# Optimization experiments

Measured on AMD Instinct MI355X. Metric: run time of the kernel, lower is better.

## Reference

```python
import jax, jax.numpy as jnp
import numpy as np
import math

XLEN, YLEN, B = 2048, 1024, 8
XD, YD, HD, YOUT = 1024, 1024, 512, 1024


def setup_inputs() -> dict:
    key = jax.random.key(0)
    ks = jax.random.split(key, 12)

    def lin(kw, kb, out_d, in_d):
        s = 1.0 / math.sqrt(in_d)
        w = jax.random.uniform(kw, (out_d, in_d), jnp.float32, -s, s)
        b = jax.random.uniform(kb, (out_d,), jnp.float32, -s, s)
        return w, b

    Xk_w, Xk_b = lin(ks[0], ks[1], HD, XD)
    Xv_w, Xv_b = lin(ks[2], ks[3], HD, XD)
    Yq_w, Yq_b = lin(ks[4], ks[5], HD, YD)
    Yw_w, Yw_b = lin(ks[6], ks[7], YOUT, YD + HD)

    X = jax.random.normal(ks[8], (XLEN, B, XD), jnp.float32)
    Y = jax.random.normal(ks[9], (YLEN, B, YD), jnp.float32)
    alignment = jax.random.normal(ks[10], (B, YLEN, XLEN), jnp.float32)
    X_pad_mask = jax.random.bernoulli(ks[11], 0.1, (B, YLEN, XLEN))  # True -> mask out
    align_w = jnp.zeros((1,), jnp.float32)  # nn.Parameter([0])

    return {"X": X, "Y": Y, "alignment": alignment, "X_pad_mask": X_pad_mask,
            "Xk_w": Xk_w, "Xk_b": Xk_b, "Xv_w": Xv_w, "Xv_b": Xv_b,
            "Yq_w": Yq_w, "Yq_b": Yq_b, "Yw_w": Yw_w, "Yw_b": Yw_b,
            "align_w": align_w}


def reference(X, Y, alignment, X_pad_mask, Xk_w, Xk_b, Xv_w, Xv_b,
              Yq_w, Yq_b, Yw_w, Yw_b, align_w):
    FMAX = jnp.finfo(X.dtype).max
    # projections (torch Linear: x @ W.T + b)
    xk = X @ Xk_w.T + Xk_b                     # (x, b, hd)
    yq = Y @ Yq_w.T + Yq_b                     # (y, b, hd)
    # scaled cross-attention logits
    logit = jnp.einsum('xbd,ybd->byx', xk, yq) / math.sqrt(xk.shape[-1])
    # gated alignment bias + clamp
    logit = logit + jax.nn.sigmoid(align_w[0]) * alignment
    logit = jnp.maximum(logit, -FMAX)
    # pad-mask additive fill (-FMAX) then clamp (matches masked_fill + add + clamp)
    logit = jnp.maximum(logit + jnp.where(X_pad_mask, -FMAX, 0.0), -FMAX)
    attn = jax.nn.softmax(logit, axis=-1)      # (b, y, x); dropout = identity (eval)
    xv = X @ Xv_w.T + Xv_b                     # (x, b, hd)
    attn_feat = jnp.einsum('byx,xbh->ybh', attn, xv)  # (y, b, hd)
    concat = jnp.concatenate([Y, attn_feat], axis=-1)  # (y, b, yd+hd)
    return concat @ Yw_w.T + Yw_b              # (y, b, y_outdim)
```

## Files before the change

kernel.cpp:

```cpp
#include <hip/hip_runtime.h>


#define FMAXF 3.402823466e38f

typedef __attribute__((ext_vector_type(8))) __bf16 bf16x8;
typedef __attribute__((ext_vector_type(4))) float f32x4;

static __device__ __forceinline__ short f2b(float f) {
  union { float f; unsigned u; } x; x.f = f;
  unsigned r = (x.u + 0x7FFFu + ((x.u >> 16) & 1u)) >> 16;
  return (short)r;
}
static __device__ __forceinline__ float b2f(short s) {
  union { unsigned u; float f; } x; x.u = ((unsigned)(unsigned short)s) << 16;
  return x.f;
}

static __device__ __forceinline__ void gl_lds16(const short* g, short* l) {
  __builtin_amdgcn_global_load_lds(
      (const __attribute__((address_space(1))) void*)g,
      (__attribute__((address_space(3))) void*)l, 16, 0, 0);
}


struct EpiKV {
  short* xk; short* xv; const float* kb; const float* vb;
  __device__ void operator()(int bz, int m, int n, float v) const {
    int b = m & 7; long x = m >> 3;
    if (n < 512) {
      xk[((long)b * 2048 + x) * 512 + n] = f2b(v + kb[n]);
    } else {
      xv[((long)b * 2048 + x) * 512 + (n - 512)] = f2b(v + vb[n - 512]);
    }
  }
};

struct EpiYq {
  short* out; const float* bias;
  __device__ void operator()(int bz, int m, int n, float v) const {
    out[(((long)(m & 7)) * 1024 + (m >> 3)) * 512 + n] = f2b(v + bias[n]);
  }
};

struct EpiLogit {
  short* out; const float* align; const int* mask; const float* alw;
  __device__ void operator()(int bz, int m, int n, float v) const {
    long idx = ((long)bz * 1024 + m) * 2048 + n;
    float g = 1.0f / (1.0f + __expf(-alw[0]));
    v = v * 0.04419417382415922f + g * align[idx];
    if (mask[idx]) v = -FMAXF;
    out[idx] = f2b(v);
  }
};

struct EpiConcat {
  short* out;
  __device__ void operator()(int bz, int m, int n, float v) const {
    out[((long)m * 8 + bz) * 1536 + 1024 + n] = f2b(v);
  }
};

struct EpiOut {
  float* out; const float* bias;
  __device__ void operator()(int bz, int m, int n, float v) const {
    out[(long)m * 1024 + n] = v + bias[n];
  }
};

template <typename Epi>
__global__ __launch_bounds__(256) void gemm128(
    const short* __restrict__ A, long sAb, int lda,
    const short* __restrict__ B, long sBb, int ldb,
    int K, Epi epi) {
  __shared__ short As[128 * 32];
  __shared__ short Bs[128 * 32];

  const int tid = threadIdx.x;
  const int lane = tid & 63, wave = tid >> 6;
  const int bz = blockIdx.z;
  const int m0 = blockIdx.x * 128;
  const int n0 = blockIdx.y * 128;

  const int rr = lane >> 2;
  const int cc = (lane & 3) * 8;
  const int row0 = wave * 32;
  const short* Ag0 = A + (long)bz * sAb + (long)(m0 + row0 + rr) * lda + cc;
  const short* Ag1 = Ag0 + (long)16 * lda;
  const short* Bg0 = B + (long)bz * sBb + (long)(n0 + row0 + rr) * ldb + cc;
  const short* Bg1 = Bg0 + (long)16 * ldb;
  short* Al0 = As + row0 * 32;
  short* Al1 = As + (row0 + 16) * 32;
  short* Bl0 = Bs + row0 * 32;
  short* Bl1 = Bs + (row0 + 16) * 32;

  const int wm = (wave & 1) * 64, wn = (wave >> 1) * 64;
  const int quad = lane >> 4, l16 = lane & 15;

  f32x4 acc[4][4] = {};

  for (int k0 = 0; k0 < K; k0 += 32) {
    gl_lds16(Ag0 + k0, Al0);
    gl_lds16(Ag1 + k0, Al1);
    gl_lds16(Bg0 + k0, Bl0);
    gl_lds16(Bg1 + k0, Bl1);
    __syncthreads();

    union { int4 v; bf16x8 f; } a[4], b[4];
#pragma unroll
    for (int i = 0; i < 4; i++) {
      a[i].v = *(const int4*)(As + (wm + i * 16 + l16) * 32 + quad * 8);
      b[i].v = *(const int4*)(Bs + (wn + i * 16 + l16) * 32 + quad * 8);
    }
#pragma unroll
    for (int i = 0; i < 4; i++)
#pragma unroll
      for (int j = 0; j < 4; j++)
        acc[i][j] = __builtin_amdgcn_mfma_f32_16x16x32_bf16(a[i].f, b[j].f,
                                                            acc[i][j], 0, 0, 0);
    __syncthreads();
  }

#pragma unroll
  for (int i = 0; i < 4; i++)
#pragma unroll
    for (int j = 0; j < 4; j++)
#pragma unroll
      for (int r = 0; r < 4; r++)
        epi(bz, m0 + wm + i * 16 + quad * 4 + r, n0 + wn + j * 16 + l16,
            acc[i][j][r]);
}

__global__ __launch_bounds__(256) void cvt_f32_bf16(const float* __restrict__ in,
                                                    short* __restrict__ out,
                                                    long n4) {
  long i = (long)blockIdx.x * 256 + threadIdx.x;
  if (i >= n4) return;
  float4 f = ((const float4*)in)[i];
  union { short s[4]; long long v; } o;
  o.s[0] = f2b(f.x); o.s[1] = f2b(f.y); o.s[2] = f2b(f.z); o.s[3] = f2b(f.w);
  ((long long*)out)[i] = o.v;
}

__global__ __launch_bounds__(256) void cvt_y_concat(const float* __restrict__ in,
                                                    short* __restrict__ out) {
  long idx = (long)blockIdx.x * 256 + threadIdx.x;
  long row = idx >> 8;
  int c = (int)(idx & 255) << 2;
  float4 f = *(const float4*)(in + row * 1024 + c);
  union { short s[4]; unsigned long long v; } o;
  o.s[0] = f2b(f.x); o.s[1] = f2b(f.y); o.s[2] = f2b(f.z); o.s[3] = f2b(f.w);
  *(unsigned long long*)(out + row * 1536 + c) = o.v;
}

__global__ __launch_bounds__(256) void transpose_xv(const short* __restrict__ xv,
                                                    short* __restrict__ xvt) {
  __shared__ short t[32][36];
  const int b = blockIdx.z;
  const long x0 = (long)blockIdx.x * 32, h0 = (long)blockIdx.y * 32;
  const int r = threadIdx.x >> 3, c = (threadIdx.x & 7) * 4;
  const short* src = xv + ((long)b * 2048 + x0 + r) * 512 + h0 + c;
  *(int2*)&t[r][c] = *(const int2*)src;
  __syncthreads();
  union { short s[4]; int2 v; } o;
  o.s[0] = t[c + 0][r]; o.s[1] = t[c + 1][r];
  o.s[2] = t[c + 2][r]; o.s[3] = t[c + 3][r];
  short* dst = xvt + ((long)b * 512 + h0 + r) * 2048 + x0 + c;
  *(int2*)dst = o.v;
}

__global__ __launch_bounds__(256) void softmax_rows(short* logits) {
  const long row = blockIdx.x;
  short* p = logits + row * 2048;
  const int tid = threadIdx.x;

  union { short s[8]; int4 v; } d;
  d.v = *(const int4*)(p + tid * 8);
  float vals[8];
  float mx = -FMAXF;
#pragma unroll
  for (int i = 0; i < 8; i++) { vals[i] = b2f(d.s[i]); mx = fmaxf(mx, vals[i]); }
#pragma unroll
  for (int off = 32; off; off >>= 1) mx = fmaxf(mx, __shfl_xor(mx, off));
  __shared__ float redm[4], reds[4];
  if ((tid & 63) == 0) redm[tid >> 6] = mx;
  __syncthreads();
  mx = fmaxf(fmaxf(redm[0], redm[1]), fmaxf(redm[2], redm[3]));

  float s = 0.0f;
#pragma unroll
  for (int i = 0; i < 8; i++) { vals[i] = __expf(vals[i] - mx); s += vals[i]; }
#pragma unroll
  for (int off = 32; off; off >>= 1) s += __shfl_xor(s, off);
  if ((tid & 63) == 0) reds[tid >> 6] = s;
  __syncthreads();
  s = reds[0] + reds[1] + reds[2] + reds[3];
  float inv = 1.0f / s;
#pragma unroll
  for (int i = 0; i < 8; i++) d.s[i] = f2b(vals[i] * inv);
  *(int4*)(p + tid * 8) = d.v;
}


extern "C" void kernel_launch(void* const* d_in, const int* in_sizes, int n_in,
                              void* d_out, int out_size, void* d_ws, size_t ws_size,
                              hipStream_t stream) {
  const float* X    = (const float*)d_in[0];
  const float* Y    = (const float*)d_in[1];
  const float* alig = (const float*)d_in[2];
  const int*   mask = (const int*)d_in[3];
  const float* Xk_w = (const float*)d_in[4];
  const float* Xk_b = (const float*)d_in[5];
  const float* Xv_w = (const float*)d_in[6];
  const float* Xv_b = (const float*)d_in[7];
  const float* Yq_w = (const float*)d_in[8];
  const float* Yq_b = (const float*)d_in[9];
  const float* Yw_w = (const float*)d_in[10];
  const float* Yw_b = (const float*)d_in[11];
  const float* alw  = (const float*)d_in[12];
  float* out = (float*)d_out;

  char* ws = (char*)d_ws;
  short* xbf    = (short*)(ws + 0);
  short* logits = (short*)(ws + 0);
  short* xk     = (short*)(ws + 33554432);
  short* xv     = (short*)(ws + 50331648);
  short* xvt    = (short*)(ws + 67108864);
  short* yq     = (short*)(ws + 83886080);
  short* concat = (short*)(ws + 92274688);
  short* wkv    = (short*)(ws + 117440512);
  short* wyq    = (short*)(ws + 119537664);
  short* wyw    = (short*)(ws + 120586240);

  cvt_f32_bf16<<<16384, 256, 0, stream>>>(X, xbf, 4194304);
  cvt_y_concat<<<8192, 256, 0, stream>>>(Y, concat);
  cvt_f32_bf16<<<512, 256, 0, stream>>>(Xk_w, wkv, 131072);
  cvt_f32_bf16<<<512, 256, 0, stream>>>(Xv_w, wkv + 512 * 1024, 131072);
  cvt_f32_bf16<<<512, 256, 0, stream>>>(Yq_w, wyq, 131072);
  cvt_f32_bf16<<<1536, 256, 0, stream>>>(Yw_w, wyw, 393216);

  gemm128<EpiKV><<<dim3(128, 8, 1), 256, 0, stream>>>(
      xbf, 0, 1024, wkv, 0, 1024, 1024, EpiKV{xk, xv, Xk_b, Xv_b});

  gemm128<EpiYq><<<dim3(64, 4, 1), 256, 0, stream>>>(
      concat, 0, 1536, wyq, 0, 1024, 1024, EpiYq{yq, Yq_b});

  transpose_xv<<<dim3(64, 16, 8), 256, 0, stream>>>(xv, xvt);

  gemm128<EpiLogit><<<dim3(8, 16, 8), 256, 0, stream>>>(
      yq, (long)1024 * 512, 512, xk, (long)2048 * 512, 512, 512,
      EpiLogit{logits, alig, mask, alw});

  softmax_rows<<<8192, 256, 0, stream>>>(logits);

  gemm128<EpiConcat><<<dim3(8, 4, 8), 256, 0, stream>>>(
      logits, (long)1024 * 2048, 2048, xvt, (long)512 * 2048, 2048, 2048,
      EpiConcat{concat});

  gemm128<EpiOut><<<dim3(64, 8, 1), 256, 0, stream>>>(
      concat, 0, 1536, wyw, 0, 1536, 1536, EpiOut{out, Yw_b});
}
```

Before: 482.7 us.

## Move alignment/mask bias into softmax, add XCD-aware tile mapping and 64-row tiles

Moves the alignment scaling, sigmoid gate and pad-mask fill out of the logit GEMM epilogue and into the softmax kernel. There they are read with vectorized float4/int4 loads instead of strided scalar accesses per MFMA output. The GEMM is generalised to a single shared-memory buffer holding both A and B tiles, with a 1D block index remapped so consecutive M tiles land on the same XCD. It also adds a 64-row M tile variant, giving more blocks for the smaller Yq and attention-value GEMMs. The risk is that the logits are now rounded to bf16 before the scale and bias are applied, which slightly changes numerics.

Result: faster. 459.4 us (-4.8%).

```diff
diff --git a/kernel.cpp b/kernel.cpp
--- a/kernel.cpp
+++ b/kernel.cpp
@@ -43,13 +43,9 @@
 };
 
 struct EpiLogit {
-  short* out; const float* align; const int* mask; const float* alw;
-  __device__ void operator()(int bz, int m, int n, float v) const {
-    long idx = ((long)bz * 1024 + m) * 2048 + n;
-    float g = 1.0f / (1.0f + __expf(-alw[0]));
-    v = v * 0.04419417382415922f + g * align[idx];
-    if (mask[idx]) v = -FMAXF;
-    out[idx] = f2b(v);
+  short* out;
+  __device__ void operator()(int bz, int m, int n, float v) const {
+    out[((long)bz * 1024 + m) * 2048 + n] = f2b(v);
   }
 };
 
@@ -67,67 +63,73 @@
   }
 };
 
-template <typename Epi>
-__global__ __launch_bounds__(256) void gemm128(
+template <int TM, typename Epi>
+__global__ __launch_bounds__(256) void gemm_mt(
     const short* __restrict__ A, long sAb, int lda,
     const short* __restrict__ B, long sBb, int ldb,
-    int K, Epi epi) {
-  __shared__ short As[128 * 32];
-  __shared__ short Bs[128 * 32];
+    int K, int tlog, Epi epi) {
+  constexpr int R = TM + 128;
+  constexpr int SEGS = R / 64;
+  __shared__ short S[R * 32];
 
   const int tid = threadIdx.x;
   const int lane = tid & 63, wave = tid >> 6;
   const int bz = blockIdx.z;
-  const int m0 = blockIdx.x * 128;
-  const int n0 = blockIdx.y * 128;
-
-  const int rr = lane >> 2;
-  const int cc = (lane & 3) * 8;
-  const int row0 = wave * 32;
-  const short* Ag0 = A + (long)bz * sAb + (long)(m0 + row0 + rr) * lda + cc;
-  const short* Ag1 = Ag0 + (long)16 * lda;
-  const short* Bg0 = B + (long)bz * sBb + (long)(n0 + row0 + rr) * ldb + cc;
-  const short* Bg1 = Bg0 + (long)16 * ldb;
-  short* Al0 = As + row0 * 32;
-  short* Al1 = As + (row0 + 16) * 32;
-  short* Bl0 = Bs + row0 * 32;
-  short* Bl1 = Bs + (row0 + 16) * 32;
-
-  const int wm = (wave & 1) * 64, wn = (wave >> 1) * 64;
+
+  const int id = blockIdx.x;
+  const int xcd = id & 7;
+  const int r = id >> 3;
+  const int n0 = (r & ((1 << tlog) - 1)) * 128;
+  const int m0 = (((r >> tlog) << 3) + xcd) * TM;
+
+  const short* gp[SEGS];
+#pragma unroll
+  for (int t = 0; t < SEGS; t++) {
+    int seg = t * 256 + tid;
+    int row = seg >> 2, col = (seg & 3) * 8;
+    gp[t] = (row < TM)
+                ? A + (long)bz * sAb + (long)(m0 + row) * lda + col
+                : B + (long)bz * sBb + (long)(n0 + row - TM) * ldb + col;
+  }
+
+  const int wm = (TM == 128) ? (wave & 1) * 64 : 0;
+  const int wn = (TM == 128) ? (wave >> 1) * 64 : wave * 32;
+  constexpr int MI = 4;
+  constexpr int MJ = (TM == 128) ? 4 : 2;
   const int quad = lane >> 4, l16 = lane & 15;
 
-  f32x4 acc[4][4] = {};
+  f32x4 acc[MI][MJ] = {};
 
   for (int k0 = 0; k0 < K; k0 += 32) {
-    gl_lds16(Ag0 + k0, Al0);
-    gl_lds16(Ag1 + k0, Al1);
-    gl_lds16(Bg0 + k0, Bl0);
-    gl_lds16(Bg1 + k0, Bl1);
+#pragma unroll
+    for (int t = 0; t < SEGS; t++)
+      gl_lds16(gp[t] + k0, S + (t * 256 + tid) * 8);
     __syncthreads();
 
-    union { int4 v; bf16x8 f; } a[4], b[4];
-#pragma unroll
-    for (int i = 0; i < 4; i++) {
-      a[i].v = *(const int4*)(As + (wm + i * 16 + l16) * 32 + quad * 8);
-      b[i].v = *(const int4*)(Bs + (wn + i * 16 + l16) * 32 + quad * 8);
-    }
-#pragma unroll
-    for (int i = 0; i < 4; i++)
-#pragma unroll
-      for (int j = 0; j < 4; j++)
+    union { int4 v; bf16x8 f; } a[MI], b[MJ];
+#pragma unroll
+    for (int i = 0; i < MI; i++)
+      a[i].v = *(const int4*)(S + (wm + i * 16 + l16) * 32 + quad * 8);
+#pragma unroll
+    for (int j = 0; j < MJ; j++)
+      b[j].v = *(const int4*)(S + (TM + wn + j * 16 + l16) * 32 + quad * 8);
+#pragma unroll
+    for (int i = 0; i < MI; i++)
+#pragma unroll
+      for (int j = 0; j < MJ; j++)
         acc[i][j] = __builtin_amdgcn_mfma_f32_16x16x32_bf16(a[i].f, b[j].f,
                                                             acc[i][j], 0, 0, 0);
     __syncthreads();
   }
 
 #pragma unroll
-  for (int i = 0; i < 4; i++)
-#pragma unroll
-    for (int j = 0; j < 4; j++)
-#pragma unroll
-      for (int r = 0; r < 4; r++)
-        epi(bz, m0 + wm + i * 16 + quad * 4 + r, n0 + wn + j * 16 + l16,
-            acc[i][j][r]);
+  for (int i = 0; i < MI; i++)
+#pragma unroll
+    for (int j = 0; j < MJ; j++)
+#pragma unroll
+      for (int r4 = 0; r4 < 4; r4++)
+        epi(bz, m0 + wm + i * 16 + quad * 4 + r4, n0 + wn + j * 16 + l16,
+            acc[i][j][r4]);
 }
 
 __global__ __launch_bounds__(256) void cvt_f32_bf16(const float* __restrict__ in,
@@ -168,20 +170,40 @@
   *(int2*)dst = o.v;
 }
 
-__global__ __launch_bounds__(256) void softmax_rows(short* logits) {
+__global__ __launch_bounds__(256) void softmax_rows(short* __restrict__ logits,
+                                                    const float* __restrict__ align,
+                                                    const int* __restrict__ mask,
+                                                    const float* __restrict__ alw) {
   const long row = blockIdx.x;
-  short* p = logits + row * 2048;
-  const int tid = threadIdx.x;
+  const long base = row * 2048 + threadIdx.x * 8;
+  short* p = logits + base;
+  const float g = 1.0f / (1.0f + __expf(-alw[0]));
+  const float scale = 0.04419417382415922f;
 
   union { short s[8]; int4 v; } d;
-  d.v = *(const int4*)(p + tid * 8);
+  d.v = *(const int4*)p;
+  float4 al0 = *(const float4*)(align + base);
+  float4 al1 = *(const float4*)(align + base + 4);
+  int4 mk0 = *(const int4*)(mask + base);
+  int4 mk1 = *(const int4*)(mask + base + 4);
+
   float vals[8];
+  vals[0] = mk0.x ? -FMAXF : b2f(d.s[0]) * scale + g * al0.x;
+  vals[1] = mk0.y ? -FMAXF : b2f(d.s[1]) * scale + g * al0.y;
+  vals[2] = mk0.z ? -FMAXF : b2f(d.s[2]) * scale + g * al0.z;
+  vals[3] = mk0.w ? -FMAXF : b2f(d.s[3]) * scale + g * al0.w;
+  vals[4] = mk1.x ? -FMAXF : b2f(d.s[4]) * scale + g * al1.x;
+  vals[5] = mk1.y ? -FMAXF : b2f(d.s[5]) * scale + g * al1.y;
+  vals[6] = mk1.z ? -FMAXF : b2f(d.s[6]) * scale + g * al1.z;
+  vals[7] = mk1.w ? -FMAXF : b2f(d.s[7]) * scale + g * al1.w;
+
   float mx = -FMAXF;
 #pragma unroll
-  for (int i = 0; i < 8; i++) { vals[i] = b2f(d.s[i]); mx = fmaxf(mx, vals[i]); }
+  for (int i = 0; i < 8; i++) mx = fmaxf(mx, vals[i]);
 #pragma unroll
   for (int off = 32; off; off >>= 1) mx = fmaxf(mx, __shfl_xor(mx, off));
   __shared__ float redm[4], reds[4];
+  const int tid = threadIdx.x;
   if ((tid & 63) == 0) redm[tid >> 6] = mx;
   __syncthreads();
   mx = fmaxf(fmaxf(redm[0], redm[1]), fmaxf(redm[2], redm[3]));
@@ -197,7 +219,7 @@
   float inv = 1.0f / s;
 #pragma unroll
   for (int i = 0; i < 8; i++) d.s[i] = f2b(vals[i] * inv);
-  *(int4*)(p + tid * 8) = d.v;
+  *(int4*)p = d.v;
 }
 
 
@@ -238,24 +260,24 @@
   cvt_f32_bf16<<<512, 256, 0, stream>>>(Yq_w, wyq, 131072);
   cvt_f32_bf16<<<1536, 256, 0, stream>>>(Yw_w, wyw, 393216);
 
-  gemm128<EpiKV><<<dim3(128, 8, 1), 256, 0, stream>>>(
-      xbf, 0, 1024, wkv, 0, 1024, 1024, EpiKV{xk, xv, Xk_b, Xv_b});
-
-  gemm128<EpiYq><<<dim3(64, 4, 1), 256, 0, stream>>>(
-      concat, 0, 1536, wyq, 0, 1024, 1024, EpiYq{yq, Yq_b});
+  gemm_mt<128, EpiKV><<<dim3(1024, 1, 1), 256, 0, stream>>>(
+      xbf, 0, 1024, wkv, 0, 1024, 1024, 3, EpiKV{xk, xv, Xk_b, Xv_b});
+
+  gemm_mt<64, EpiYq><<<dim3(512, 1, 1), 256, 0, stream>>>(
+      concat, 0, 1536, wyq, 0, 1024, 1024, 2, EpiYq{yq, Yq_b});
 
   transpose_xv<<<dim3(64, 16, 8), 256, 0, stream>>>(xv, xvt);
 
-  gemm128<EpiLogit><<<dim3(8, 16, 8), 256, 0, stream>>>(
-      yq, (long)1024 * 512, 512, xk, (long)2048 * 512, 512, 512,
-      EpiLogit{logits, alig, mask, alw});
-
-  softmax_rows<<<8192, 256, 0, stream>>>(logits);
-
-  gemm128<EpiConcat><<<dim3(8, 4, 8), 256, 0, stream>>>(
-      logits, (long)1024 * 2048, 2048, xvt, (long)512 * 2048, 2048, 2048,
+  gemm_mt<128, EpiLogit><<<dim3(128, 1, 8), 256, 0, stream>>>(
+      yq, (long)1024 * 512, 512, xk, (long)2048 * 512, 512, 512, 4,
+      EpiLogit{logits});
+
+  softmax_rows<<<8192, 256, 0, stream>>>(logits, alig, mask, alw);
+
+  gemm_mt<64, EpiConcat><<<dim3(64, 1, 8), 256, 0, stream>>>(
+      logits, (long)1024 * 2048, 2048, xvt, (long)512 * 2048, 2048, 2048, 2,
       EpiConcat{concat});
 
-  gemm128<EpiOut><<<dim3(64, 8, 1), 256, 0, stream>>>(
-      concat, 0, 1536, wyw, 0, 1536, 1536, EpiOut{out, Yw_b});
-}
+  gemm_mt<128, EpiOut><<<dim3(512, 1, 1), 256, 0, stream>>>(
+      concat, 0, 1536, wyw, 0, 1536, 1536, 3, EpiOut{out, Yw_b});
+}
```
